# Kernel tuning notes

Measured on AMD Instinct MI355X. Metric: run time of the kernel, lower is better.

Reference implementation:

```python
import jax, jax.numpy as jnp
import numpy as np

D = 1024      # embed_dim
H = 16        # num_heads
HD = D // H   # head_dim


def setup_inputs() -> dict:
    key = jax.random.key(0)
    ks = jax.random.split(key, 9)
    s = 0.02
    x = jax.random.normal(ks[0], (8, 1024, D), dtype=jnp.float32)
    # Per-head Q/K/V linears, torch Linear layout [out, in] -> stacked [H, HD, D]
    Wq = jax.random.normal(ks[1], (H, HD, D), dtype=jnp.float32) * s
    Wk = jax.random.normal(ks[2], (H, HD, D), dtype=jnp.float32) * s
    Wv = jax.random.normal(ks[3], (H, HD, D), dtype=jnp.float32) * s
    bq = jax.random.normal(ks[4], (H, HD), dtype=jnp.float32) * s
    bk = jax.random.normal(ks[5], (H, HD), dtype=jnp.float32) * s
    bv = jax.random.normal(ks[6], (H, HD), dtype=jnp.float32) * s
    Wo = jax.random.normal(ks[7], (D, D), dtype=jnp.float32) * s
    bo = jax.random.normal(ks[8], (D,), dtype=jnp.float32) * s
    return {"x": x, "Wq": Wq, "Wk": Wk, "Wv": Wv,
            "bq": bq, "bk": bk, "bv": bv, "Wo": Wo, "bo": bo}


def reference(x, Wq, Wk, Wv, bq, bk, bv, Wo, bo):
    # Batched per-head projections: [B,S,D] x [H,HD,D] -> [B,H,S,HD]
    q = jnp.einsum('bsd,hkd->bhsk', x, Wq) + bq[None, :, None, :]
    k = jnp.einsum('bsd,hkd->bhsk', x, Wk) + bk[None, :, None, :]
    v = jnp.einsum('bsd,hkd->bhsk', x, Wv) + bv[None, :, None, :]
    scores = jnp.einsum('bhqk,bhsk->bhqs', q, k) / jnp.sqrt(jnp.float32(HD))
    probs = jax.nn.softmax(scores, axis=-1)          # [B,H,S,S]
    attn = jnp.einsum('bhqs,bhsk->bhqk', probs, v)   # [B,H,S,HD]
    # Concat heads along feature dim -> [B,S,D]
    B, _, S, _ = attn.shape
    concat = jnp.transpose(attn, (0, 2, 1, 3)).reshape(B, S, D)
    out = jnp.einsum('bsd,ed->bse', concat, Wo) + bo  # output projection
    return out
```

## Files before the change

### kernel.cpp

```cpp
#include <hip/hip_runtime.h>
#include <stdint.h>
#include <stddef.h>


typedef short bf16x8 __attribute__((ext_vector_type(8)));
typedef float f32x4  __attribute__((ext_vector_type(4)));
typedef unsigned short u16x8 __attribute__((ext_vector_type(8)));
typedef unsigned short u16x4 __attribute__((ext_vector_type(4)));

#define MFMA16 __builtin_amdgcn_mfma_f32_16x16x32_bf16

typedef const void __attribute__((address_space(1)))* gas1_t;
typedef void __attribute__((address_space(3)))* las3_t;

static __device__ __forceinline__ void gload16(const void* g, void* l) {
  __builtin_amdgcn_global_load_lds((gas1_t)g, (las3_t)l, 16, 0, 0);
}

static __device__ __forceinline__ unsigned short f2bf(float f) {
  union { float f; unsigned int u; } v; v.f = f;
  unsigned int r = v.u + 0x7fffu + ((v.u >> 16) & 1u);
  return (unsigned short)(r >> 16);
}

__global__ __launch_bounds__(256) void cast_all(
    const float* __restrict__ x, const float* __restrict__ Wq,
    const float* __restrict__ Wk, const float* __restrict__ Wv,
    const float* __restrict__ Wo,
    unsigned short* __restrict__ xb, unsigned short* __restrict__ wqkv,
    unsigned short* __restrict__ wob) {
  int base = (blockIdx.x * 256 + threadIdx.x) * 4;
  const float* s; unsigned short* d;
  if (base < 8388608) { s = x + base; d = xb + base; }
  else if (base < 11534336) {
    int o = base - 8388608; int wi = o >> 20;
    const float* w = (wi == 0) ? Wq : (wi == 1) ? Wk : Wv;
    s = w + (o & 1048575); d = wqkv + o;
  } else {
    int o = base - 11534336; s = Wo + o; d = wob + o;
  }
  float4 f = *(const float4*)s;
  u16x4 r; r[0] = f2bf(f.x); r[1] = f2bf(f.y); r[2] = f2bf(f.z); r[3] = f2bf(f.w);
  *(u16x4*)d = r;
}

template <int EPI>
__global__ __launch_bounds__(256) void gemm128(
    const unsigned short* __restrict__ A, const unsigned short* __restrict__ Bm,
    float* __restrict__ Cf, const float* __restrict__ bO,
    unsigned short* __restrict__ Qo, unsigned short* __restrict__ Ko,
    unsigned short* __restrict__ Vo,
    const float* __restrict__ bq, const float* __restrict__ bk,
    const float* __restrict__ bv) {
  __shared__ __align__(16) char sm[32768];
  char* As = sm; char* Bs = sm + 16384;
  const int tid = threadIdx.x, lane = tid & 63, w = tid >> 6;
  const int wr = w >> 1, wc = w & 1;
  const int brow = blockIdx.y * 128, bcol = blockIdx.x * 128;
  const int l15 = lane & 15, g = lane >> 4;
  f32x4 acc[4][4] = {};
  for (int ks = 0; ks < 16; ++ks) {
    __syncthreads();
#pragma unroll
    for (int j = 0; j < 4; ++j) {
      int p = (w * 4 + j) * 1024 + lane * 16;
      int row = p >> 7;
      int cl = (lane & 7) ^ (row & 7);
      gload16(A + (size_t)(brow + row) * 1024 + ks * 64 + cl * 8,
              As + (w * 4 + j) * 1024);
      gload16(Bm + (size_t)(bcol + row) * 1024 + ks * 64 + cl * 8,
              Bs + (w * 4 + j) * 1024);
    }
    asm volatile("s_waitcnt vmcnt(0)" ::: "memory");
    __syncthreads();
#pragma unroll
    for (int kk = 0; kk < 2; ++kk) {
      bf16x8 af[4], bfr[4];
#pragma unroll
      for (int mi = 0; mi < 4; ++mi) {
        int row = wr * 64 + mi * 16 + l15;
        int off = (row * 128 + kk * 64 + g * 16) ^ ((row & 7) << 4);
        af[mi] = *(const bf16x8*)(As + off);
      }
#pragma unroll
      for (int ni = 0; ni < 4; ++ni) {
        int row = wc * 64 + ni * 16 + l15;
        int off = (row * 128 + kk * 64 + g * 16) ^ ((row & 7) << 4);
        bfr[ni] = *(const bf16x8*)(Bs + off);
      }
#pragma unroll
      for (int mi = 0; mi < 4; ++mi)
#pragma unroll
        for (int ni = 0; ni < 4; ++ni)
          acc[mi][ni] = MFMA16(af[mi], bfr[ni], acc[mi][ni], 0, 0, 0);
    }
  }
  if constexpr (EPI == 0) {
    const int b = brow >> 10;
#pragma unroll
    for (int ni = 0; ni < 4; ++ni) {
      int n = bcol + wc * 64 + ni * 16 + l15;
      int t = n >> 10, nh = n & 1023;
      int h = nh >> 6, hd = nh & 63;
      const float* bias = (t == 0) ? bq : (t == 1) ? bk : bv;
      float bb = bias[nh];
      float scale = (t == 0) ? 0.125f : 1.0f;
      unsigned short* dst = (t == 0) ? Qo : (t == 1) ? Ko : Vo;
      size_t basei = ((size_t)(b * 16 + h) * 1024) * 64 + hd;
#pragma unroll
      for (int mi = 0; mi < 4; ++mi)
#pragma unroll
        for (int r = 0; r < 4; ++r) {
          int m = brow + wr * 64 + mi * 16 + g * 4 + r;
          int srow = m & 1023;
          dst[basei + (size_t)srow * 64] = f2bf((acc[mi][ni][r] + bb) * scale);
        }
    }
  } else {
#pragma unroll
    for (int ni = 0; ni < 4; ++ni) {
      int n = bcol + wc * 64 + ni * 16 + l15;
      float bb = bO[n];
#pragma unroll
      for (int mi = 0; mi < 4; ++mi)
#pragma unroll
        for (int r = 0; r < 4; ++r) {
          int m = brow + wr * 64 + mi * 16 + g * 4 + r;
          Cf[(size_t)m * 1024 + n] = acc[mi][ni][r] + bb;
        }
    }
  }
}

__global__ __launch_bounds__(256) void attn_fused(
    const unsigned short* __restrict__ Qb, const unsigned short* __restrict__ Kb,
    const unsigned short* __restrict__ Vb, unsigned short* __restrict__ Cc) {
  __shared__ __align__(16) char sm[52224];
  char* Qs = sm;
  char* Ks = sm + 16384;
  char* Vt = sm + 24576;
  const int tid = threadIdx.x, lane = tid & 63, w = tid >> 6;
  char* Ps = sm + 33792 + w * 4608;
  const int l15 = lane & 15, g = lane >> 4;
  const int qt = blockIdx.x, h = blockIdx.y, b = blockIdx.z;
  const size_t hb = (size_t)(b * 16 + h) * (1024 * 64);

#pragma unroll
  for (int j = 0; j < 4; ++j) {
    int p = (w * 4 + j) * 1024 + lane * 16;
    int row = p >> 7;
    int cl = (lane & 7) ^ (row & 7);
    gload16(Qb + hb + (size_t)(qt * 128 + row) * 64 + cl * 8, Qs + (w * 4 + j) * 1024);
  }

  f32x4 acc_o[2][4] = {};
  float m_run[2] = {-1e30f, -1e30f};
  float l_run[2] = {0.f, 0.f};

  for (int c = 0; c < 16; ++c) {
    __syncthreads();
#pragma unroll
    for (int j = 0; j < 2; ++j) {
      int p = (w * 2 + j) * 1024 + lane * 16;
      int row = p >> 7;
      int cl = (lane & 7) ^ (row & 7);
      gload16(Kb + hb + (size_t)(c * 64 + row) * 64 + cl * 8, Ks + (w * 2 + j) * 1024);
    }
#pragma unroll
    for (int i = 0; i < 2; ++i) {
      int idx = tid + i * 256;
      int srow = idx >> 3, oct = idx & 7;
      u16x8 vv = *(const u16x8*)(Vb + hb + (size_t)(c * 64 + srow) * 64 + oct * 8);
#pragma unroll
      for (int jj = 0; jj < 8; ++jj)
        *(unsigned short*)(Vt + ((oct * 8 + jj) * 72 + srow) * 2) = vv[jj];
    }
    asm volatile("s_waitcnt vmcnt(0)" ::: "memory");
    __syncthreads();

    f32x4 st[4][2] = {};
#pragma unroll
    for (int kk = 0; kk < 2; ++kk) {
      bf16x8 ka[4], qf[2];
#pragma unroll
      for (int mi = 0; mi < 4; ++mi) {
        int row = mi * 16 + l15;
        int off = (row * 128 + kk * 64 + g * 16) ^ ((row & 7) << 4);
        ka[mi] = *(const bf16x8*)(Ks + off);
      }
#pragma unroll
      for (int ni = 0; ni < 2; ++ni) {
        int row = w * 32 + ni * 16 + l15;
        int off = (row * 128 + kk * 64 + g * 16) ^ ((row & 7) << 4);
        qf[ni] = *(const bf16x8*)(Qs + off);
      }
#pragma unroll
      for (int mi = 0; mi < 4; ++mi)
#pragma unroll
        for (int ni = 0; ni < 2; ++ni)
          st[mi][ni] = MFMA16(ka[mi], qf[ni], st[mi][ni], 0, 0, 0);
    }

    float corr_s[2];
#pragma unroll
    for (int ni = 0; ni < 2; ++ni) {
      float mx = -1e30f;
#pragma unroll
      for (int mi = 0; mi < 4; ++mi)
#pragma unroll
        for (int r = 0; r < 4; ++r) mx = fmaxf(mx, st[mi][ni][r]);
      mx = fmaxf(mx, __shfl_xor(mx, 16));
      mx = fmaxf(mx, __shfl_xor(mx, 32));
      float mn = fmaxf(m_run[ni], mx);
      float corr = __expf(m_run[ni] - mn);
      float sum = 0.f;
#pragma unroll
      for (int mi = 0; mi < 4; ++mi) {
        u16x4 pk;
#pragma unroll
        for (int r = 0; r < 4; ++r) {
          float e = __expf(st[mi][ni][r] - mn);
          sum += e;
          pk[r] = f2bf(e);
        }
        *(u16x4*)(Ps + ((ni * 16 + l15) * 72 + mi * 16 + g * 4) * 2) = pk;
      }
      sum += __shfl_xor(sum, 16);
      sum += __shfl_xor(sum, 32);
      l_run[ni] = l_run[ni] * corr + sum;
      m_run[ni] = mn;
      corr_s[ni] = corr;
    }

#pragma unroll
    for (int mi = 0; mi < 2; ++mi) {
      float cr[4];
#pragma unroll
      for (int r = 0; r < 4; ++r)
        cr[r] = __shfl(corr_s[mi], (lane & 48) + g * 4 + r);
#pragma unroll
      for (int nd = 0; nd < 4; ++nd)
#pragma unroll
        for (int r = 0; r < 4; ++r)
          acc_o[mi][nd][r] *= cr[r];
    }

#pragma unroll
    for (int kk = 0; kk < 2; ++kk) {
      bf16x8 pa[2], vf[4];
#pragma unroll
      for (int mi = 0; mi < 2; ++mi)
        pa[mi] = *(const bf16x8*)(Ps + (mi * 16 + l15) * 144 + kk * 64 + g * 16);
#pragma unroll
      for (int nd = 0; nd < 4; ++nd)
        vf[nd] = *(const bf16x8*)(Vt + (nd * 16 + l15) * 144 + kk * 64 + g * 16);
#pragma unroll
      for (int mi = 0; mi < 2; ++mi)
#pragma unroll
        for (int nd = 0; nd < 4; ++nd)
          acc_o[mi][nd] = MFMA16(pa[mi], vf[nd], acc_o[mi][nd], 0, 0, 0);
    }
  }

  float invl[2] = {1.f / l_run[0], 1.f / l_run[1]};
#pragma unroll
  for (int mi = 0; mi < 2; ++mi) {
    float iv[4];
#pragma unroll
    for (int r = 0; r < 4; ++r)
      iv[r] = __shfl(invl[mi], (lane & 48) + g * 4 + r);
#pragma unroll
    for (int nd = 0; nd < 4; ++nd)
#pragma unroll
      for (int r = 0; r < 4; ++r) {
        int q = qt * 128 + w * 32 + mi * 16 + g * 4 + r;
        int col = h * 64 + nd * 16 + l15;
        Cc[(size_t)(b * 1024 + q) * 1024 + col] = f2bf(acc_o[mi][nd][r] * iv[r]);
      }
  }
}

extern "C" void kernel_launch(void* const* d_in, const int* in_sizes, int n_in,
                              void* d_out, int out_size, void* d_ws, size_t ws_size,
                              hipStream_t stream) {
  const float* x  = (const float*)d_in[0];
  const float* Wq = (const float*)d_in[1];
  const float* Wk = (const float*)d_in[2];
  const float* Wv = (const float*)d_in[3];
  const float* bq = (const float*)d_in[4];
  const float* bk = (const float*)d_in[5];
  const float* bv = (const float*)d_in[6];
  const float* Wo = (const float*)d_in[7];
  const float* bo = (const float*)d_in[8];

  char* ws = (char*)d_ws;
  unsigned short* xb   = (unsigned short*)(ws);
  unsigned short* wqkv = (unsigned short*)(ws + 16777216);
  unsigned short* wob  = (unsigned short*)(ws + 23068672);
  unsigned short* Qb   = (unsigned short*)(ws + 25165824);
  unsigned short* Kb   = (unsigned short*)(ws + 41943040);
  unsigned short* Vb   = (unsigned short*)(ws + 58720256);
  unsigned short* Cc   = xb;

  cast_all<<<dim3(12288), dim3(256), 0, stream>>>(x, Wq, Wk, Wv, Wo, xb, wqkv, wob);
  gemm128<0><<<dim3(24, 64), dim3(256), 0, stream>>>(
      xb, wqkv, nullptr, nullptr, Qb, Kb, Vb, bq, bk, bv);
  attn_fused<<<dim3(8, 16, 8), dim3(256), 0, stream>>>(Qb, Kb, Vb, Cc);
  gemm128<1><<<dim3(8, 64), dim3(256), 0, stream>>>(
      Cc, wob, (float*)d_out, bo, nullptr, nullptr, nullptr, nullptr, nullptr, nullptr);
}
```

Measured before the change: 288.7 us.

## Pre-transpose V in QKV epilogue and double-buffer K/V tiles in attention

The QKV GEMM epilogue now writes V already transposed ([bh, hd, s]), so the attention kernel can stage V with async global-to-LDS loads instead of per-element transposing stores. K and V tiles are double-buffered so the next chunk's loads overlap the current chunk's compute, with one barrier per iteration. Q is held in registers rather than LDS, and the P·V MFMA is transposed so output and corrections need no cross-lane shuffles. A 1D grid and an occupancy hint of 3 blocks/CU are added. The risk is register pressure from the extra state and uncoalesced strided writes of V in the GEMM epilogue.

```diff
diff --git a/kernel.cpp b/kernel.cpp
--- a/kernel.cpp
+++ b/kernel.cpp
@@ -104,17 +104,30 @@
       int h = nh >> 6, hd = nh & 63;
       const float* bias = (t == 0) ? bq : (t == 1) ? bk : bv;
       float bb = bias[nh];
-      float scale = (t == 0) ? 0.125f : 1.0f;
-      unsigned short* dst = (t == 0) ? Qo : (t == 1) ? Ko : Vo;
-      size_t basei = ((size_t)(b * 16 + h) * 1024) * 64 + hd;
-#pragma unroll
-      for (int mi = 0; mi < 4; ++mi)
-#pragma unroll
-        for (int r = 0; r < 4; ++r) {
-          int m = brow + wr * 64 + mi * 16 + g * 4 + r;
-          int srow = m & 1023;
-          dst[basei + (size_t)srow * 64] = f2bf((acc[mi][ni][r] + bb) * scale);
+      if (t == 2) {
+        size_t vtb = ((size_t)(b * 16 + h) * 64 + hd) * 1024;
+#pragma unroll
+        for (int mi = 0; mi < 4; ++mi) {
+          int m0 = brow + wr * 64 + mi * 16 + g * 4;
+          int srow0 = m0 & 1023;
+          u16x4 vv;
+#pragma unroll
+          for (int r = 0; r < 4; ++r) vv[r] = f2bf(acc[mi][ni][r] + bb);
+          *(u16x4*)(Vo + vtb + srow0) = vv;
         }
+      } else {
+        float scale = (t == 0) ? 0.125f : 1.0f;
+        unsigned short* dst = (t == 0) ? Qo : Ko;
+        size_t basei = ((size_t)(b * 16 + h) * 1024) * 64 + hd;
+#pragma unroll
+        for (int mi = 0; mi < 4; ++mi)
+#pragma unroll
+          for (int r = 0; r < 4; ++r) {
+            int m = brow + wr * 64 + mi * 16 + g * 4 + r;
+            int srow = m & 1023;
+            dst[basei + (size_t)srow * 64] = f2bf((acc[mi][ni][r] + bb) * scale);
+          }
+      }
     }
   } else {
 #pragma unroll
@@ -132,73 +145,70 @@
   }
 }
 
-__global__ __launch_bounds__(256) void attn_fused(
+__global__ __launch_bounds__(256, 3) void attn_fused(
     const unsigned short* __restrict__ Qb, const unsigned short* __restrict__ Kb,
-    const unsigned short* __restrict__ Vb, unsigned short* __restrict__ Cc) {
-  __shared__ __align__(16) char sm[52224];
-  char* Qs = sm;
-  char* Ks = sm + 16384;
-  char* Vt = sm + 24576;
+    const unsigned short* __restrict__ VtG, unsigned short* __restrict__ Cc) {
+  __shared__ __align__(16) char sm[49152];
+  char* Ks = sm;
+  char* Vt = sm + 16384;
   const int tid = threadIdx.x, lane = tid & 63, w = tid >> 6;
-  char* Ps = sm + 33792 + w * 4608;
+  char* Ps = sm + 32768 + w * 4096;
   const int l15 = lane & 15, g = lane >> 4;
-  const int qt = blockIdx.x, h = blockIdx.y, b = blockIdx.z;
-  const size_t hb = (size_t)(b * 16 + h) * (1024 * 64);
-
-#pragma unroll
-  for (int j = 0; j < 4; ++j) {
-    int p = (w * 4 + j) * 1024 + lane * 16;
-    int row = p >> 7;
-    int cl = (lane & 7) ^ (row & 7);
-    gload16(Qb + hb + (size_t)(qt * 128 + row) * 64 + cl * 8, Qs + (w * 4 + j) * 1024);
-  }
-
-  f32x4 acc_o[2][4] = {};
-  float m_run[2] = {-1e30f, -1e30f};
-  float l_run[2] = {0.f, 0.f};
-
-  for (int c = 0; c < 16; ++c) {
-    __syncthreads();
+  const int id = blockIdx.x;
+  const int qt = id >> 7, bh = id & 127;
+  const size_t hb = (size_t)bh * (1024 * 64);
+
+  bf16x8 qreg[2][2];
+#pragma unroll
+  for (int kk = 0; kk < 2; ++kk)
+#pragma unroll
+    for (int ni = 0; ni < 2; ++ni) {
+      int q = qt * 128 + w * 32 + ni * 16 + l15;
+      qreg[kk][ni] = *(const bf16x8*)(Qb + hb + (size_t)q * 64 + kk * 32 + g * 8);
+    }
+
+  auto stage = [&](int c, int buf) {
 #pragma unroll
     for (int j = 0; j < 2; ++j) {
       int p = (w * 2 + j) * 1024 + lane * 16;
       int row = p >> 7;
       int cl = (lane & 7) ^ (row & 7);
-      gload16(Kb + hb + (size_t)(c * 64 + row) * 64 + cl * 8, Ks + (w * 2 + j) * 1024);
-    }
-#pragma unroll
-    for (int i = 0; i < 2; ++i) {
-      int idx = tid + i * 256;
-      int srow = idx >> 3, oct = idx & 7;
-      u16x8 vv = *(const u16x8*)(Vb + hb + (size_t)(c * 64 + srow) * 64 + oct * 8);
-#pragma unroll
-      for (int jj = 0; jj < 8; ++jj)
-        *(unsigned short*)(Vt + ((oct * 8 + jj) * 72 + srow) * 2) = vv[jj];
-    }
-    asm volatile("s_waitcnt vmcnt(0)" ::: "memory");
-    __syncthreads();
+      gload16(Kb + hb + (size_t)(c * 64 + row) * 64 + cl * 8,
+              Ks + buf * 8192 + (w * 2 + j) * 1024);
+      gload16(VtG + hb + (size_t)row * 1024 + c * 64 + cl * 8,
+              Vt + buf * 8192 + (w * 2 + j) * 1024);
+    }
+  };
+
+  stage(0, 0);
+  asm volatile("s_waitcnt vmcnt(0)" ::: "memory");
+  __syncthreads();
+
+  f32x4 acc[4][2] = {};
+  float m_run[2] = {-1e30f, -1e30f};
+  float l_run[2] = {0.f, 0.f};
+
+  for (int c = 0; c < 16; ++c) {
+    const int cur = c & 1;
+    if (c < 15) stage(c + 1, cur ^ 1);
+    const char* Kc = Ks + cur * 8192;
+    const char* Vc = Vt + cur * 8192;
 
     f32x4 st[4][2] = {};
 #pragma unroll
     for (int kk = 0; kk < 2; ++kk) {
-      bf16x8 ka[4], qf[2];
+      bf16x8 ka[4];
 #pragma unroll
       for (int mi = 0; mi < 4; ++mi) {
         int row = mi * 16 + l15;
         int off = (row * 128 + kk * 64 + g * 16) ^ ((row & 7) << 4);
-        ka[mi] = *(const bf16x8*)(Ks + off);
-      }
-#pragma unroll
-      for (int ni = 0; ni < 2; ++ni) {
-        int row = w * 32 + ni * 16 + l15;
-        int off = (row * 128 + kk * 64 + g * 16) ^ ((row & 7) << 4);
-        qf[ni] = *(const bf16x8*)(Qs + off);
+        ka[mi] = *(const bf16x8*)(Kc + off);
       }
 #pragma unroll
       for (int mi = 0; mi < 4; ++mi)
 #pragma unroll
         for (int ni = 0; ni < 2; ++ni)
-          st[mi][ni] = MFMA16(ka[mi], qf[ni], st[mi][ni], 0, 0, 0);
+          st[mi][ni] = MFMA16(ka[mi], qreg[kk][ni], st[mi][ni], 0, 0, 0);
     }
 
     float corr_s[2];
@@ -214,6 +224,8 @@
       float mn = fmaxf(m_run[ni], mx);
       float corr = __expf(m_run[ni] - mn);
       float sum = 0.f;
+      const int q = ni * 16 + l15;
+      const int rbase = q * 128, sw = (q & 7) << 4;
 #pragma unroll
       for (int mi = 0; mi < 4; ++mi) {
         u16x4 pk;
@@ -223,7 +235,7 @@
           sum += e;
           pk[r] = f2bf(e);
         }
-        *(u16x4*)(Ps + ((ni * 16 + l15) * 72 + mi * 16 + g * 4) * 2) = pk;
+        *(u16x4*)(Ps + ((rbase + (mi * 16 + g * 4) * 2) ^ sw)) = pk;
       }
       sum += __shfl_xor(sum, 16);
       sum += __shfl_xor(sum, 32);
@@ -233,50 +245,52 @@
     }
 
 #pragma unroll
-    for (int mi = 0; mi < 2; ++mi) {
-      float cr[4];
-#pragma unroll
-      for (int r = 0; r < 4; ++r)
-        cr[r] = __shfl(corr_s[mi], (lane & 48) + g * 4 + r);
+    for (int nd = 0; nd < 4; ++nd)
+#pragma unroll
+      for (int ni = 0; ni < 2; ++ni)
+#pragma unroll
+        for (int r = 0; r < 4; ++r)
+          acc[nd][ni][r] *= corr_s[ni];
+
+#pragma unroll
+    for (int kk = 0; kk < 2; ++kk) {
+      bf16x8 vf[4], pa[2];
+#pragma unroll
+      for (int nd = 0; nd < 4; ++nd) {
+        int row = nd * 16 + l15;
+        int off = (row * 128 + kk * 64 + g * 16) ^ ((row & 7) << 4);
+        vf[nd] = *(const bf16x8*)(Vc + off);
+      }
+#pragma unroll
+      for (int ni = 0; ni < 2; ++ni) {
+        int q = ni * 16 + l15;
+        int off = (q * 128 + kk * 64 + g * 16) ^ ((q & 7) << 4);
+        pa[ni] = *(const bf16x8*)(Ps + off);
+      }
 #pragma unroll
       for (int nd = 0; nd < 4; ++nd)
 #pragma unroll
-        for (int r = 0; r < 4; ++r)
-          acc_o[mi][nd][r] *= cr[r];
-    }
-
-#pragma unroll
-    for (int kk = 0; kk < 2; ++kk) {
-      bf16x8 pa[2], vf[4];
-#pragma unroll
-      for (int mi = 0; mi < 2; ++mi)
-        pa[mi] = *(const bf16x8*)(Ps + (mi * 16 + l15) * 144 + kk * 64 + g * 16);
-#pragma unroll
-      for (int nd = 0; nd < 4; ++nd)
-        vf[nd] = *(const bf16x8*)(Vt + (nd * 16 + l15) * 144 + kk * 64 + g * 16);
-#pragma unroll
-      for (int mi = 0; mi < 2; ++mi)
-#pragma unroll
-        for (int nd = 0; nd < 4; ++nd)
-          acc_o[mi][nd] = MFMA16(pa[mi], vf[nd], acc_o[mi][nd], 0, 0, 0);
-    }
-  }
-
+        for (int ni = 0; ni < 2; ++ni)
+          acc[nd][ni] = MFMA16(vf[nd], pa[ni], acc[nd][ni], 0, 0, 0);
+    }
+
+    asm volatile("s_waitcnt vmcnt(0)" ::: "memory");
+    __syncthreads();
+  }
+
+  const int b = bh >> 4, h = bh & 15;
   float invl[2] = {1.f / l_run[0], 1.f / l_run[1]};
 #pragma unroll
-  for (int mi = 0; mi < 2; ++mi) {
-    float iv[4];
-#pragma unroll
-    for (int r = 0; r < 4; ++r)
-      iv[r] = __shfl(invl[mi], (lane & 48) + g * 4 + r);
-#pragma unroll
-    for (int nd = 0; nd < 4; ++nd)
-#pragma unroll
-      for (int r = 0; r < 4; ++r) {
-        int q = qt * 128 + w * 32 + mi * 16 + g * 4 + r;
-        int col = h * 64 + nd * 16 + l15;
-        Cc[(size_t)(b * 1024 + q) * 1024 + col] = f2bf(acc_o[mi][nd][r] * iv[r]);
-      }
+  for (int ni = 0; ni < 2; ++ni) {
+    int q = qt * 128 + w * 32 + ni * 16 + l15;
+    size_t rowb = (size_t)(b * 1024 + q) * 1024 + h * 64;
+#pragma unroll
+    for (int nd = 0; nd < 4; ++nd) {
+      u16x4 o;
+#pragma unroll
+      for (int r = 0; r < 4; ++r) o[r] = f2bf(acc[nd][ni][r] * invl[ni]);
+      *(u16x4*)(Cc + rowb + nd * 16 + g * 4) = o;
+    }
   }
 }
 
@@ -299,13 +313,13 @@
   unsigned short* wob  = (unsigned short*)(ws + 23068672);
   unsigned short* Qb   = (unsigned short*)(ws + 25165824);
   unsigned short* Kb   = (unsigned short*)(ws + 41943040);
-  unsigned short* Vb   = (unsigned short*)(ws + 58720256);
+  unsigned short* VtG  = (unsigned short*)(ws + 58720256);
   unsigned short* Cc   = xb;
 
   cast_all<<<dim3(12288), dim3(256), 0, stream>>>(x, Wq, Wk, Wv, Wo, xb, wqkv, wob);
   gemm128<0><<<dim3(24, 64), dim3(256), 0, stream>>>(
-      xb, wqkv, nullptr, nullptr, Qb, Kb, Vb, bq, bk, bv);
-  attn_fused<<<dim3(8, 16, 8), dim3(256), 0, stream>>>(Qb, Kb, Vb, Cc);
+      xb, wqkv, nullptr, nullptr, Qb, Kb, VtG, bq, bk, bv);
+  attn_fused<<<dim3(1024), dim3(256), 0, stream>>>(Qb, Kb, VtG, Cc);
   gemm128<1><<<dim3(8, 64), dim3(256), 0, stream>>>(
       Cc, wob, (float*)d_out, bo, nullptr, nullptr, nullptr, nullptr, nullptr, nullptr);
 }
```

After: 255.7 us. 11.4% less time.
